# Kernel tuning notes

Measured on AMD Instinct MI355X. Metric: run time of the kernel, lower is better.

The kernel has to match this reference:

```python
import jax, jax.numpy as jnp
import numpy as np

BN_EPS = 1e-5  # torch BatchNorm1d default


def setup_inputs() -> dict:
    key = jax.random.key(0)
    k = jax.random.split(key, 5)
    B, D, L = 4096, 4096, 4  # batch, width, num layers (3 hidden + 1 output)
    x = jax.random.normal(k[0], (B, D), dtype=jnp.float32)
    # Per-layer Linear weights stored as [L, in, out]; scaled like xavier-ish init.
    W = jax.random.normal(k[1], (L, D, D), dtype=jnp.float32) * (1.0 / np.sqrt(D))
    b = jax.random.normal(k[2], (L, D), dtype=jnp.float32) * 0.01
    gamma = jax.random.uniform(k[3], (L, D), dtype=jnp.float32, minval=0.5, maxval=1.5)
    beta = jax.random.normal(k[4], (L, D), dtype=jnp.float32) * 0.1
    return {"x": x, "W": W, "b": b, "gamma": gamma, "beta": beta}


def _layer(h, W_l, b_l, gamma_l, beta_l):
    # one big GEMM replaces the per-neuron GEMV loop + stack
    h = h @ W_l + b_l  # [B, out]
    # BatchNorm1d, training mode: biased batch stats over the batch dim
    mu = jnp.mean(h, axis=0)
    var = jnp.var(h, axis=0)
    h = (h - mu) * jax.lax.rsqrt(var + BN_EPS) * gamma_l + beta_l
    return jax.nn.relu(h)


def reference(x, W, b, gamma, beta):
    out = x
    for l in range(W.shape[0]):  # small fixed layer count
        out = _layer(out, W[l], b[l], gamma[l], beta[l])
    # nn.Softmax(dim=0): softmax over the batch dimension, as in the original
    return jax.nn.softmax(out, axis=0)
```

## Files before the change

kernel.cpp:

```cpp
#include <hip/hip_runtime.h>
#include <stdint.h>

#define DIMD 4096
#define DIMB 4096
#define NLAYER 4
#define NT (DIMD / 64)

typedef unsigned short u16;
typedef __attribute__((ext_vector_type(4))) float f32x4;
typedef __attribute__((ext_vector_type(8))) __bf16 bf16x8;

__device__ __forceinline__ u16 f2bf(float f) {
    union { float f; uint32_t u; } v; v.f = f;
    return (u16)((v.u + 0x7fffu + ((v.u >> 16) & 1u)) >> 16);
}

__global__ void k_cvt(const float* __restrict__ in, u16* __restrict__ out) {
    int i = (blockIdx.x * 256 + threadIdx.x) * 4;
    float4 v = *reinterpret_cast<const float4*>(in + i);
    ushort4 r;
    r.x = f2bf(v.x); r.y = f2bf(v.y); r.z = f2bf(v.z); r.w = f2bf(v.w);
    *reinterpret_cast<ushort4*>(out + i) = r;
}

__global__ void k_trans(const float* __restrict__ W, u16* __restrict__ Wt) {
    __shared__ float tile[32][33];
    int tx = threadIdx.x & 31, ty = threadIdx.x >> 5;
    int n0 = blockIdx.x * 32, k0 = blockIdx.y * 32;
    #pragma unroll
    for (int r = 0; r < 4; ++r)
        tile[ty + r * 8][tx] = W[(size_t)(k0 + ty + r * 8) * DIMD + n0 + tx];
    __syncthreads();
    #pragma unroll
    for (int r = 0; r < 4; ++r) {
        int nn = ty + r * 8;
        Wt[(size_t)(n0 + nn) * DIMD + k0 + tx] = f2bf(tile[tx][nn]);
    }
}

#define GLD(g, l) __builtin_amdgcn_global_load_lds( \
    (__attribute__((address_space(1))) void*)(g),   \
    (__attribute__((address_space(3))) void*)(l), 16, 0, 0)

__global__ __launch_bounds__(512, 2) void k_gemm(
        const u16* __restrict__ A, const u16* __restrict__ Bt,
        const float* __restrict__ bias, float* __restrict__ C,
        float* __restrict__ csum, float* __restrict__ csum2) {
    __shared__ __attribute__((aligned(16))) u16 As[2 * 256 * 64];
    __shared__ __attribute__((aligned(16))) u16 Bs[2 * 256 * 64];
    const int tid = threadIdx.x;
    const int lane = tid & 63, wv = tid >> 6;
    const int wm = wv >> 2, wn = wv & 3;
    const int bm = blockIdx.y, bn = blockIdx.x;
    const int lr = lane & 15, lk = lane >> 4;

    const int r0 = tid >> 3;
    const int cswz = (tid & 7) ^ (r0 & 7);
    const u16* gA = A  + (size_t)(bm * 256 + r0) * DIMD + cswz * 8;
    const u16* gB = Bt + (size_t)(bn * 256 + r0) * DIMD + cswz * 8;

#define STAGE_A(h, t, buf) do { \
    const u16* _s = gA + (size_t)(h) * 128 * DIMD + (size_t)(t) * 64; \
    u16* _d = As + (buf) * 16384 + (h) * 8192 + wv * 512; \
    GLD(_s, _d); GLD(_s + (size_t)64 * DIMD, _d + 4096); \
} while (0)
#define STAGE_B(h, t, buf) do { \
    const u16* _s = gB + (size_t)(h) * 128 * DIMD + (size_t)(t) * 64; \
    u16* _d = Bs + (buf) * 16384 + (h) * 8192 + wv * 512; \
    GLD(_s, _d); GLD(_s + (size_t)64 * DIMD, _d + 4096); \
} while (0)

    int aoff[4][2], boff[2][2];
    #pragma unroll
    for (int mf = 0; mf < 4; ++mf)
        #pragma unroll
        for (int ks = 0; ks < 2; ++ks) {
            int row = wm * 128 + mf * 16 + lr;
            aoff[mf][ks] = row * 64 + ((ks * 4 + lk) ^ (row & 7)) * 8;
        }
    #pragma unroll
    for (int nf = 0; nf < 2; ++nf)
        #pragma unroll
        for (int ks = 0; ks < 2; ++ks) {
            int row = wn * 64 + nf * 16 + lr;
            boff[nf][ks] = row * 64 + ((ks * 4 + lk) ^ (row & 7)) * 8;
        }

    f32x4 acc[8][4] = {};
    bf16x8 a[4][2], b0[2][2], b1[2][2];

    STAGE_A(0, 0, 0); STAGE_A(1, 0, 0); STAGE_B(0, 0, 0); STAGE_B(1, 0, 0);
    STAGE_A(0, 1, 1);
    asm volatile("s_waitcnt vmcnt(2)" ::: "memory");
    __builtin_amdgcn_s_barrier();

    for (int t = 0; t < NT; ++t) {
        const int cur = t & 1, nxt = cur ^ 1;
        const u16* Ab = As + cur * 16384;
        const u16* Bb = Bs + cur * 16384;

        #pragma unroll
        for (int mf = 0; mf < 4; ++mf)
            #pragma unroll
            for (int ks = 0; ks < 2; ++ks)
                a[mf][ks] = *reinterpret_cast<const bf16x8*>(Ab + aoff[mf][ks]);
        #pragma unroll
        for (int nf = 0; nf < 2; ++nf)
            #pragma unroll
            for (int ks = 0; ks < 2; ++ks)
                b0[nf][ks] = *reinterpret_cast<const bf16x8*>(Bb + boff[nf][ks]);
        if (t + 1 < NT) STAGE_A(1, t + 1, nxt);
        __builtin_amdgcn_s_barrier();
        asm volatile("s_waitcnt lgkmcnt(0)" ::: "memory");
        __builtin_amdgcn_s_setprio(1);
        #pragma unroll
        for (int mf = 0; mf < 4; ++mf)
            #pragma unroll
            for (int nf = 0; nf < 2; ++nf)
                #pragma unroll
                for (int ks = 0; ks < 2; ++ks)
                    acc[mf][nf] = __builtin_amdgcn_mfma_f32_16x16x32_bf16(
                        a[mf][ks], b0[nf][ks], acc[mf][nf], 0, 0, 0);
        __builtin_amdgcn_s_setprio(0);
        __builtin_amdgcn_s_barrier();

        #pragma unroll
        for (int nf = 0; nf < 2; ++nf)
            #pragma unroll
            for (int ks = 0; ks < 2; ++ks)
                b1[nf][ks] = *reinterpret_cast<const bf16x8*>(Bb + 2048 + boff[nf][ks]);
        if (t + 1 < NT) STAGE_B(0, t + 1, nxt);
        __builtin_amdgcn_s_barrier();
        asm volatile("s_waitcnt lgkmcnt(0)" ::: "memory");
        __builtin_amdgcn_s_setprio(1);
        #pragma unroll
        for (int mf = 0; mf < 4; ++mf)
            #pragma unroll
            for (int nf = 0; nf < 2; ++nf)
                #pragma unroll
                for (int ks = 0; ks < 2; ++ks)
                    acc[mf][2 + nf] = __builtin_amdgcn_mfma_f32_16x16x32_bf16(
                        a[mf][ks], b1[nf][ks], acc[mf][2 + nf], 0, 0, 0);
        __builtin_amdgcn_s_setprio(0);
        __builtin_amdgcn_s_barrier();

        #pragma unroll
        for (int mf = 0; mf < 4; ++mf)
            #pragma unroll
            for (int ks = 0; ks < 2; ++ks)
                a[mf][ks] = *reinterpret_cast<const bf16x8*>(Ab + 4096 + aoff[mf][ks]);
        if (t + 1 < NT) STAGE_B(1, t + 1, nxt);
        __builtin_amdgcn_s_barrier();
        asm volatile("s_waitcnt lgkmcnt(0)" ::: "memory");
        __builtin_amdgcn_s_setprio(1);
        #pragma unroll
        for (int mf = 0; mf < 4; ++mf)
            #pragma unroll
            for (int nf = 0; nf < 2; ++nf)
                #pragma unroll
                for (int ks = 0; ks < 2; ++ks)
                    acc[4 + mf][2 + nf] = __builtin_amdgcn_mfma_f32_16x16x32_bf16(
                        a[mf][ks], b1[nf][ks], acc[4 + mf][2 + nf], 0, 0, 0);
        __builtin_amdgcn_s_setprio(0);
        __builtin_amdgcn_s_barrier();

        if (t + 2 < NT) STAGE_A(0, t + 2, cur);
        __builtin_amdgcn_s_setprio(1);
        #pragma unroll
        for (int mf = 0; mf < 4; ++mf)
            #pragma unroll
            for (int nf = 0; nf < 2; ++nf)
                #pragma unroll
                for (int ks = 0; ks < 2; ++ks)
                    acc[4 + mf][nf] = __builtin_amdgcn_mfma_f32_16x16x32_bf16(
                        a[mf][ks], b0[nf][ks], acc[4 + mf][nf], 0, 0, 0);
        __builtin_amdgcn_s_setprio(0);
        if (t + 2 < NT) asm volatile("s_waitcnt vmcnt(2)" ::: "memory");
        else            asm volatile("s_waitcnt vmcnt(0)" ::: "memory");
        __builtin_amdgcn_s_barrier();
    }

    #pragma unroll
    for (int nh = 0; nh < 2; ++nh)
        #pragma unroll
        for (int nf = 0; nf < 2; ++nf) {
            int n = nh * 2 + nf;
            int col = bn * 256 + wn * 64 + nh * 32 + nf * 16 + lr;
            float bv = bias[col];
            float s1 = 0.f, s2 = 0.f;
            #pragma unroll
            for (int m = 0; m < 8; ++m) {
                int rbase = bm * 256 + wm * 128 + (m >> 2) * 64 + (m & 3) * 16 + lk * 4;
                #pragma unroll
                for (int r = 0; r < 4; ++r) {
                    float v = acc[m][n][r] + bv;
                    C[(size_t)(rbase + r) * DIMD + col] = v;
                    s1 += v; s2 += v * v;
                }
            }
            s1 += __shfl_xor(s1, 16); s1 += __shfl_xor(s1, 32);
            s2 += __shfl_xor(s2, 16); s2 += __shfl_xor(s2, 32);
            if (lk == 0) {
                atomicAdd(&csum[col], s1);
                atomicAdd(&csum2[col], s2);
            }
        }
#undef STAGE_A
#undef STAGE_B
}

__global__ void k_bnfin(float* __restrict__ sum, float* __restrict__ sum2,
                        const float* __restrict__ gamma, const float* __restrict__ beta) {
    int j = blockIdx.x * 256 + threadIdx.x;
    float mu = sum[j] * (1.0f / DIMB);
    float var = sum2[j] * (1.0f / DIMB) - mu * mu;
    float rstd = rsqrtf(var + 1e-5f);
    float s = gamma[j] * rstd;
    sum[j] = s;
    sum2[j] = beta[j] - mu * s;
}

__global__ void k_norm(const float* __restrict__ H, const float* __restrict__ s,
                       const float* __restrict__ t, u16* __restrict__ o) {
    int j = blockIdx.x * 256 + threadIdx.x;
    int i0 = blockIdx.y * 128;
    float sj = s[j], tj = t[j];
    for (int i = i0; i < i0 + 128; ++i) {
        float v = fmaxf(H[(size_t)i * DIMD + j] * sj + tj, 0.0f);
        o[(size_t)i * DIMD + j] = f2bf(v);
    }
}

__global__ void k_normexp(float* __restrict__ H, const float* __restrict__ s,
                          const float* __restrict__ t, float* __restrict__ esum) {
    int j = blockIdx.x * 256 + threadIdx.x;
    int i0 = blockIdx.y * 128;
    float sj = s[j], tj = t[j];
    float acc = 0.f;
    for (int i = i0; i < i0 + 128; ++i) {
        float v = fmaxf(H[(size_t)i * DIMD + j] * sj + tj, 0.0f);
        float e = __expf(v);
        H[(size_t)i * DIMD + j] = e;
        acc += e;
    }
    atomicAdd(&esum[j], acc);
}

__global__ void k_div(float* __restrict__ H, const float* __restrict__ esum) {
    int i = (blockIdx.x * 256 + threadIdx.x) * 4;
    float4 v = *reinterpret_cast<const float4*>(H + i);
    const float4 e = *reinterpret_cast<const float4*>(esum + (i & (DIMD - 1)));
    v.x /= e.x; v.y /= e.y; v.z /= e.z; v.w /= e.w;
    *reinterpret_cast<float4*>(H + i) = v;
}

extern "C" void kernel_launch(void* const* d_in, const int* in_sizes, int n_in,
                              void* d_out, int out_size, void* d_ws, size_t ws_size,
                              hipStream_t stream) {
    (void)in_sizes; (void)n_in; (void)out_size; (void)ws_size;
    const float* x     = (const float*)d_in[0];
    const float* W     = (const float*)d_in[1];
    const float* b     = (const float*)d_in[2];
    const float* gamma = (const float*)d_in[3];
    const float* beta  = (const float*)d_in[4];
    float* out = (float*)d_out;

    char* ws = (char*)d_ws;
    u16*  Abf   = (u16*)ws;
    u16*  Wt    = (u16*)(ws + (size_t)32 * 1024 * 1024);
    float* stats = (float*)(ws + (size_t)64 * 1024 * 1024);
    hipMemsetAsync(stats, 0, (4 * 8192 + 4096) * sizeof(float), stream);

    k_cvt<<<DIMB * DIMD / 1024, 256, 0, stream>>>(x, Abf);

    for (int l = 0; l < NLAYER; ++l) {
        k_trans<<<dim3(128, 128), 256, 0, stream>>>(W + (size_t)l * DIMD * DIMD, Wt);
        float* sum = stats + l * 8192;
        float* sum2 = sum + 4096;
        k_gemm<<<dim3(16, 16), 512, 0, stream>>>(Abf, Wt, b + l * DIMD, out, sum, sum2);
        k_bnfin<<<16, 256, 0, stream>>>(sum, sum2, gamma + l * DIMD, beta + l * DIMD);
        if (l < NLAYER - 1)
            k_norm<<<dim3(16, 32), 256, 0, stream>>>(out, sum, sum2, Abf);
        else
            k_normexp<<<dim3(16, 32), 256, 0, stream>>>(out, sum, sum2, stats + 32768);
    }
    k_div<<<DIMB * DIMD / 1024, 256, 0, stream>>>(out, stats + 32768);
}
```

Before: 789.9 us.

## Prefetch whole GEMM tiles two steps ahead and vectorize weight transpose

The GEMM main loop now loads both A and B tiles for iteration t+2 into the buffer just consumed, instead of spreading t+1 loads across phases. The prologue preloads two full tiles, and the loop waits with vmcnt(8) so one full tile stays in flight during compute. This is meant to hide more global-load latency, at the cost of a burstier issue pattern and tighter buffer-reuse ordering. Separately, the transpose kernel moves to 64x64 tiles with float4 loads and ushort4 stores to cut the number of memory transactions.

```diff
diff --git a/kernel.cpp b/kernel.cpp
--- a/kernel.cpp
+++ b/kernel.cpp
@@ -24,17 +24,29 @@
 }
 
 __global__ void k_trans(const float* __restrict__ W, u16* __restrict__ Wt) {
-    __shared__ float tile[32][33];
-    int tx = threadIdx.x & 31, ty = threadIdx.x >> 5;
-    int n0 = blockIdx.x * 32, k0 = blockIdx.y * 32;
-    #pragma unroll
-    for (int r = 0; r < 4; ++r)
-        tile[ty + r * 8][tx] = W[(size_t)(k0 + ty + r * 8) * DIMD + n0 + tx];
+    __shared__ float tile[64][65];
+    const int t = threadIdx.x;
+    const int n0 = blockIdx.x * 64, k0 = blockIdx.y * 64;
+    const int kr = t >> 4, c4 = (t & 15) * 4;
+    #pragma unroll
+    for (int r = 0; r < 4; ++r) {
+        float4 v = *reinterpret_cast<const float4*>(W + (size_t)(k0 + kr + r * 16) * DIMD + n0 + c4);
+        tile[kr + r * 16][c4 + 0] = v.x;
+        tile[kr + r * 16][c4 + 1] = v.y;
+        tile[kr + r * 16][c4 + 2] = v.z;
+        tile[kr + r * 16][c4 + 3] = v.w;
+    }
     __syncthreads();
+    const int nr = t >> 4, k4 = (t & 15) * 4;
     #pragma unroll
     for (int r = 0; r < 4; ++r) {
-        int nn = ty + r * 8;
-        Wt[(size_t)(n0 + nn) * DIMD + k0 + tx] = f2bf(tile[tx][nn]);
+        int n = nr + r * 16;
+        ushort4 o;
+        o.x = f2bf(tile[k4 + 0][n]);
+        o.y = f2bf(tile[k4 + 1][n]);
+        o.z = f2bf(tile[k4 + 2][n]);
+        o.w = f2bf(tile[k4 + 3][n]);
+        *reinterpret_cast<ushort4*>(Wt + (size_t)(n0 + n) * DIMD + k0 + k4) = o;
     }
 }
 
@@ -89,15 +101,16 @@
     f32x4 acc[8][4] = {};
     bf16x8 a[4][2], b0[2][2], b1[2][2];
 
-    STAGE_A(0, 0, 0); STAGE_A(1, 0, 0); STAGE_B(0, 0, 0); STAGE_B(1, 0, 0);
-    STAGE_A(0, 1, 1);
-    asm volatile("s_waitcnt vmcnt(2)" ::: "memory");
+    STAGE_B(0, 0, 0); STAGE_B(1, 0, 0); STAGE_A(0, 0, 0); STAGE_A(1, 0, 0);
+    STAGE_B(0, 1, 1); STAGE_B(1, 1, 1); STAGE_A(0, 1, 1); STAGE_A(1, 1, 1);
+    asm volatile("s_waitcnt vmcnt(8)" ::: "memory");
     __builtin_amdgcn_s_barrier();
 
     for (int t = 0; t < NT; ++t) {
-        const int cur = t & 1, nxt = cur ^ 1;
+        const int cur = t & 1;
         const u16* Ab = As + cur * 16384;
         const u16* Bb = Bs + cur * 16384;
+        const bool pf = (t + 2 < NT);
 
         #pragma unroll
         for (int mf = 0; mf < 4; ++mf)
@@ -109,7 +122,6 @@
             #pragma unroll
             for (int ks = 0; ks < 2; ++ks)
                 b0[nf][ks] = *reinterpret_cast<const bf16x8*>(Bb + boff[nf][ks]);
-        if (t + 1 < NT) STAGE_A(1, t + 1, nxt);
         __builtin_amdgcn_s_barrier();
         asm volatile("s_waitcnt lgkmcnt(0)" ::: "memory");
         __builtin_amdgcn_s_setprio(1);
@@ -129,7 +141,6 @@
             #pragma unroll
             for (int ks = 0; ks < 2; ++ks)
                 b1[nf][ks] = *reinterpret_cast<const bf16x8*>(Bb + 2048 + boff[nf][ks]);
-        if (t + 1 < NT) STAGE_B(0, t + 1, nxt);
         __builtin_amdgcn_s_barrier();
         asm volatile("s_waitcnt lgkmcnt(0)" ::: "memory");
         __builtin_amdgcn_s_setprio(1);
@@ -149,7 +160,7 @@
             #pragma unroll
             for (int ks = 0; ks < 2; ++ks)
                 a[mf][ks] = *reinterpret_cast<const bf16x8*>(Ab + 4096 + aoff[mf][ks]);
-        if (t + 1 < NT) STAGE_B(1, t + 1, nxt);
+        if (pf) { STAGE_B(0, t + 2, cur); STAGE_B(1, t + 2, cur); }
         __builtin_amdgcn_s_barrier();
         asm volatile("s_waitcnt lgkmcnt(0)" ::: "memory");
         __builtin_amdgcn_s_setprio(1);
@@ -164,7 +175,7 @@
         __builtin_amdgcn_s_setprio(0);
         __builtin_amdgcn_s_barrier();
 
-        if (t + 2 < NT) STAGE_A(0, t + 2, cur);
+        if (pf) { STAGE_A(0, t + 2, cur); STAGE_A(1, t + 2, cur); }
         __builtin_amdgcn_s_setprio(1);
         #pragma unroll
         for (int mf = 0; mf < 4; ++mf)
@@ -175,8 +186,8 @@
                     acc[4 + mf][nf] = __builtin_amdgcn_mfma_f32_16x16x32_bf16(
                         a[mf][ks], b0[nf][ks], acc[4 + mf][nf], 0, 0, 0);
         __builtin_amdgcn_s_setprio(0);
-        if (t + 2 < NT) asm volatile("s_waitcnt vmcnt(2)" ::: "memory");
-        else            asm volatile("s_waitcnt vmcnt(0)" ::: "memory");
+        if (pf) asm volatile("s_waitcnt vmcnt(8)" ::: "memory");
+        else    asm volatile("s_waitcnt vmcnt(0)" ::: "memory");
         __builtin_amdgcn_s_barrier();
     }
 
@@ -274,7 +285,7 @@
     k_cvt<<<DIMB * DIMD / 1024, 256, 0, stream>>>(x, Abf);
 
     for (int l = 0; l < NLAYER; ++l) {
-        k_trans<<<dim3(128, 128), 256, 0, stream>>>(W + (size_t)l * DIMD * DIMD, Wt);
+        k_trans<<<dim3(64, 64), 256, 0, stream>>>(W + (size_t)l * DIMD * DIMD, Wt);
         float* sum = stats + l * 8192;
         float* sum2 = sum + 4096;
         k_gemm<<<dim3(16, 16), 512, 0, stream>>>(Abf, Wt, b + l * DIMD, out, sum, sum2);
```

New measurement: 733.7 us. 7.1% less time.
